# Kernel tuning notes

Hardware: AMD Instinct MI355X
Metric: run time of the kernel (lower is better)

## Reference

```python
import jax, jax.numpy as jnp
import numpy as np

B = 32768          # RL batch (many parallel env steps)
N = 12             # robot graph nodes (1 torso + 11 joint nodes)
D = 64             # node embedding dim
TORSO_DIM = 6
JOINT_DIM = 2
N_JOINTS = 11
OBS_DIM = TORSO_DIM + N_JOINTS * JOINT_DIM  # 28


def _build_adj_norm():
    # Ant-like tree: torso node 0, four legs of ~3 nodes each; edge_index was
    # built with self_loop=True and GCNConv uses add_self_loops=False, so we
    # symmetric-normalize (A + I).
    A = np.zeros((N, N), np.float32)
    edges = [(0, 1), (1, 2), (2, 3), (0, 4), (4, 5), (5, 6),
             (0, 7), (7, 8), (8, 9), (0, 10), (10, 11)]
    for i, j in edges:
        A[i, j] = 1.0
        A[j, i] = 1.0
    A += np.eye(N, dtype=np.float32)
    dinv = 1.0 / np.sqrt(A.sum(1))
    return jnp.asarray(A * dinv[:, None] * dinv[None, :])


def setup_inputs() -> dict:
    key = jax.random.key(0)
    ks = jax.random.split(key, 12)

    def w(k, shape):
        fan_in = shape[0]
        return jax.random.normal(k, shape, jnp.float32) / np.sqrt(fan_in)

    return {
        "observations": jax.random.normal(ks[0], (B, OBS_DIM), jnp.float32),
        "adj_norm": _build_adj_norm(),
        "w_in_torso": w(ks[1], (TORSO_DIM, D)), "b_in_torso": jnp.zeros((D,), jnp.float32),
        "w_in_joint": w(ks[2], (JOINT_DIM, D)), "b_in_joint": jnp.zeros((D,), jnp.float32),
        "w_gp1": w(ks[3], (D, D)), "b_gp1": jnp.zeros((D,), jnp.float32),
        "w_gp2": w(ks[4], (D, D)), "b_gp2": jnp.zeros((D,), jnp.float32),
        "w_gv1": w(ks[5], (D, D)), "b_gv1": jnp.zeros((D,), jnp.float32),
        "w_gv2": w(ks[6], (D, D)), "b_gv2": jnp.zeros((D,), jnp.float32),
        "w_pol1": w(ks[7], (D, D)), "b_pol1": jnp.zeros((D,), jnp.float32),
        "w_pol2": w(ks[8], (D, 1)), "b_pol2": jnp.zeros((1,), jnp.float32),
        "w_val1": w(ks[9], (N * D, D)), "b_val1": jnp.zeros((D,), jnp.float32),
        "w_val2": w(ks[10], (D, 1)), "b_val2": jnp.zeros((1,), jnp.float32),
    }


def reference(observations, adj_norm,
              w_in_torso, b_in_torso, w_in_joint, b_in_joint,
              w_gp1, b_gp1, w_gp2, b_gp2,
              w_gv1, b_gv1, w_gv2, b_gv2,
              w_pol1, b_pol1, w_pol2, b_pol2,
              w_val1, b_val1, w_val2, b_val2):
    b = observations.shape[0]
    # --- masked per-group node embedding (input model) ---
    obs_torso = observations[:, :TORSO_DIM]                              # [B,6]
    obs_joint = observations[:, TORSO_DIM:].reshape(b, N_JOINTS, JOINT_DIM)
    emb_t = jnp.tanh(obs_torso @ w_in_torso + b_in_torso)[:, None, :]    # [B,1,D]
    emb_j = jnp.tanh(jnp.einsum('bnf,fd->bnd', obs_joint, w_in_joint) + b_in_joint)
    x = jnp.concatenate([emb_t, emb_j], axis=1)                          # [B,N,D]

    # --- propagation model: GCNConv(x) = A_norm @ (x W) + b ---
    def gcn(h, W, bias):
        return jnp.einsum('nm,bmd->bnd', adj_norm, h @ W) + bias

    xp = jnp.tanh(gcn(x, w_gp1, b_gp1))
    xp = jnp.tanh(gcn(xp, w_gp2, b_gp2))                                 # policy GNN
    xv = jnp.tanh(gcn(x, w_gv1, b_gv1))
    xv = jnp.tanh(gcn(xv, w_gv2, b_gv2))                                 # value GNN

    # --- policy heads: one scalar per action (joint) node, shared group net ---
    act_emb = xp[:, 1:, :]                                               # [B,11,D]
    h = jnp.tanh(act_emb @ w_pol1 + b_pol1)
    latent_pi = (h @ w_pol2 + b_pol2)[..., 0]                            # [B,11]

    # --- value head: flatten all node embeddings ---
    flat = xv.reshape(b, N * D)                                          # [B,768]
    hv = jnp.tanh(flat @ w_val1 + b_val1)
    latent_vf = hv @ w_val2 + b_val2                                     # [B,1]
    return latent_pi, latent_vf
```

## Files before the change

### kernel.cpp

```cpp
#include <hip/hip_runtime.h>

#define NB 32768
#define NN 12
#define DD 64
#define OBSD 28
#define EPB 16
#define NSLOT 136

typedef __bf16 bf16x8 __attribute__((ext_vector_type(8)));
typedef __bf16 bf16x4 __attribute__((ext_vector_type(4)));
typedef __bf16 bf16x2 __attribute__((ext_vector_type(2)));
typedef float  f32x4  __attribute__((ext_vector_type(4)));

#define MFMA(a, b, c) __builtin_amdgcn_mfma_f32_16x16x32_bf16((a), (b), (c), 0, 0, 0)

__device__ __forceinline__ float tanh_fast(float x) {
    float e = __builtin_amdgcn_exp2f(x * 2.885390081777927f);
    float r = __builtin_amdgcn_rcpf(e + 1.f);
    return __builtin_fmaf(-2.f, r, 1.f);
}

static constexpr int AC_OFF[13] = {0,5,8,11,13,16,19,21,24,27,29,32,34};
static constexpr int AC_M[34] = {0,1,4,7,10, 0,1,2, 1,2,3, 2,3, 0,4,5, 4,5,6, 5,6, 0,7,8, 7,8,9, 8,9, 0,10,11, 10,11};
static constexpr int AC_N[34] = {0,0,0,0,0, 1,1,1, 2,2,2, 3,3, 4,4,4, 5,5,5, 6,6, 7,7,7, 8,8,8, 9,9, 10,10,10, 11,11};

__global__ __launch_bounds__(256) void prep_weights(
    const float* __restrict__ gp1, const float* __restrict__ gp2,
    const float* __restrict__ gv1, const float* __restrict__ gv2,
    const float* __restrict__ pol1, const float* __restrict__ val1,
    __bf16* __restrict__ wsb)
{
    int gid = blockIdx.x * blockDim.x + threadIdx.x;
    if (gid >= NSLOT * 64) return;
    int slot = gid >> 6, l = gid & 63;
    const float* W; int w, ks;
    if (slot < 32) {
        int m = slot >> 3;
        W = (m == 0) ? gp1 : (m == 1) ? gp2 : (m == 2) ? gv1 : gv2;
        w = (slot >> 1) & 3; ks = slot & 1;
    } else if (slot < 40) {
        W = pol1; w = (slot - 32) >> 1; ks = slot & 1;
    } else {
        int idx = slot - 40; W = val1; w = idx / 24; ks = idx % 24;
    }
    int dout = w * 16 + (l & 15);
    int k0 = ks * 32 + (l >> 4) * 8;
    bf16x8 v;
    #pragma unroll
    for (int i = 0; i < 8; ++i) v[i] = (__bf16)W[(size_t)(k0 + i) * 64 + dout];
    *(bf16x8*)(wsb + (size_t)gid * 8) = v;
}

__global__ __launch_bounds__(512, 6) void nervenet_mfma(
    const float* __restrict__ obs, const float* __restrict__ adjn,
    const float* __restrict__ w_in_t, const float* __restrict__ b_in_t,
    const float* __restrict__ w_in_j, const float* __restrict__ b_in_j,
    const float* __restrict__ b_gp1, const float* __restrict__ b_gp2,
    const float* __restrict__ b_gv1, const float* __restrict__ b_gv2,
    const float* __restrict__ b_pol1, const float* __restrict__ w_pol2, const float* __restrict__ b_pol2,
    const float* __restrict__ b_val1, const float* __restrict__ w_val2, const float* __restrict__ b_val2,
    const __bf16* __restrict__ wsb, float* __restrict__ out)
{
    __shared__ unsigned char X [NN * EPB * DD * 2];
    __shared__ unsigned char XP[NN * EPB * DD * 2];
    __shared__ float polp[4 * 11 * EPB];
    __shared__ float valp[4 * EPB];

    const int tid = threadIdx.x;
    const int l   = tid & 63;
    const int el  = l & 15;
    const int kg  = l >> 4;
    const int wv  = tid >> 6;
    const int w   = wv & 3;
    const bool isP = wv < 4;
    const int b0  = blockIdx.x * EPB;
    const int swz = (el & 7) << 4;

    float ac[34];
    #pragma unroll
    for (int i = 0; i < 34; ++i) ac[i] = adjn[AC_N[i] * 12 + AC_M[i]];

    {
        const int ee = tid & 15, fg = tid >> 4;
        const int eswz = (ee & 7) << 4;
        const float* os = obs + (size_t)(b0 + ee) * OBSD;
        f32x4 o0 = *(const f32x4*)(os);
        f32x4 o1 = *(const f32x4*)(os + 4);
        f32x4 o2 = *(const f32x4*)(os + 8);
        f32x4 o3 = *(const f32x4*)(os + 12);
        f32x4 o4 = *(const f32x4*)(os + 16);
        f32x4 o5 = *(const f32x4*)(os + 20);
        f32x4 o6 = *(const f32x4*)(os + 24);
        float tors[6] = {o0[0], o0[1], o0[2], o0[3], o1[0], o1[1]};
        float j0[11] = {o1[2], o2[0], o2[2], o3[0], o3[2], o4[0], o4[2], o5[0], o5[2], o6[0], o6[2]};
        float j1[11] = {o1[3], o2[1], o2[3], o3[1], o3[3], o4[1], o4[3], o5[1], o5[3], o6[1], o6[3]};

        float y0 = b_in_t[fg * 2], y1 = b_in_t[fg * 2 + 1];
        #pragma unroll
        for (int ff = 0; ff < 6; ++ff) {
            y0 = __builtin_fmaf(tors[ff], w_in_t[ff * DD + fg * 2], y0);
            y1 = __builtin_fmaf(tors[ff], w_in_t[ff * DD + fg * 2 + 1], y1);
        }
        bf16x2 t;
        t[0] = (__bf16)tanh_fast(y0); t[1] = (__bf16)tanh_fast(y1);
        *(bf16x2*)(&X[(0 * EPB + ee) * 128 + ((fg * 4) ^ eswz)]) = t;

        const float wj0a = w_in_j[fg * 2], wj0b = w_in_j[fg * 2 + 1];
        const float wj1a = w_in_j[DD + fg * 2], wj1b = w_in_j[DD + fg * 2 + 1];
        const float bja = b_in_j[fg * 2], bjb = b_in_j[fg * 2 + 1];
        #pragma unroll
        for (int n = 1; n < NN; ++n) {
            float ya = __builtin_fmaf(j1[n-1], wj1a, __builtin_fmaf(j0[n-1], wj0a, bja));
            float yb = __builtin_fmaf(j1[n-1], wj1b, __builtin_fmaf(j0[n-1], wj0b, bjb));
            t[0] = (__bf16)tanh_fast(ya); t[1] = (__bf16)tanh_fast(yb);
            *(bf16x2*)(&X[(n * EPB + ee) * 128 + ((fg * 4) ^ eswz)]) = t;
        }
    }

    auto rdfrag = [&](const unsigned char* buf, int n, int ks) {
        return *(const bf16x8*)(buf + (n * EPB + el) * 128 + ((ks * 64 + kg * 16) ^ swz));
    };
    auto ldws = [&](int slot) {
        return *(const bf16x8*)(wsb + ((size_t)slot * 64 + l) * 8);
    };

    f32x4 acc[NN];

    auto gcn_read = [&](const unsigned char* src, int slotbase) {
        bf16x8 wf0 = ldws(slotbase + w * 2 + 0);
        bf16x8 wf1 = ldws(slotbase + w * 2 + 1);
        #pragma unroll
        for (int n = 0; n < NN; ++n) {
            bf16x8 x0 = rdfrag(src, n, 0);
            bf16x8 x1 = rdfrag(src, n, 1);
            f32x4 a = {0.f, 0.f, 0.f, 0.f};
            a = MFMA(wf0, x0, a);
            a = MFMA(wf1, x1, a);
            acc[n] = a;
        }
    };
    auto gcn_write = [&](unsigned char* dst, const float* bias) {
        f32x4 bv = *(const f32x4*)(bias + w * 16 + kg * 4);
        #pragma unroll
        for (int n = 0; n < NN; ++n) {
            f32x4 y = bv;
            #pragma unroll
            for (int j = AC_OFF[n]; j < AC_OFF[n + 1]; ++j) {
                const float a = ac[j];
                #pragma unroll
                for (int r = 0; r < 4; ++r) y[r] = __builtin_fmaf(a, acc[AC_M[j]][r], y[r]);
            }
            bf16x4 o;
            #pragma unroll
            for (int r = 0; r < 4; ++r) o[r] = (__bf16)tanh_fast(y[r]);
            *(bf16x4*)(dst + (n * EPB + el) * 128 + (((w * 16 + kg * 4) * 2) ^ swz)) = o;
        }
    };

    unsigned char* MYBUF = isP ? XP : X;

    __syncthreads();
    gcn_read(X, isP ? 0 : 16);
    __syncthreads();
    gcn_write(MYBUF, isP ? b_gp1 : b_gv1);
    __syncthreads();
    gcn_read(MYBUF, isP ? 8 : 24);
    __syncthreads();
    gcn_write(MYBUF, isP ? b_gp2 : b_gv2);
    __syncthreads();

    {
        f32x4 bp  = *(const f32x4*)(b_pol1 + w * 16 + kg * 4);
        f32x4 wp2 = *(const f32x4*)(w_pol2 + w * 16 + kg * 4);
        bf16x8 pf0 = ldws(32 + w * 2 + 0);
        bf16x8 pf1 = ldws(32 + w * 2 + 1);
        auto pol_unit = [&](int nj) {
            bf16x8 x0 = rdfrag(XP, nj + 1, 0);
            bf16x8 x1 = rdfrag(XP, nj + 1, 1);
            f32x4 a = bp;
            a = MFMA(pf0, x0, a);
            a = MFMA(pf1, x1, a);
            float p = 0.f;
            #pragma unroll
            for (int r = 0; r < 4; ++r) p += tanh_fast(a[r]) * wp2[r];
            p += __shfl_xor(p, 16);
            p += __shfl_xor(p, 32);
            if (kg == 0) polp[w * 176 + nj * 16 + el] = p;
        };
        if (isP) {
            #pragma unroll
            for (int nj = 0; nj < 7; ++nj) pol_unit(nj);
        } else {
            #pragma unroll
            for (int nj = 7; nj < 11; ++nj) pol_unit(nj);
            f32x4 a0 = *(const f32x4*)(b_val1 + w * 16 + kg * 4);
            f32x4 a1 = {0.f, 0.f, 0.f, 0.f};
            #pragma unroll 4
            for (int ks = 0; ks < 24; ks += 2) {
                bf16x8 wf0 = ldws(40 + w * 24 + ks);
                bf16x8 wf1 = ldws(40 + w * 24 + ks + 1);
                int n = ks >> 1;
                bf16x8 xf0 = rdfrag(X, n, 0);
                bf16x8 xf1 = rdfrag(X, n, 1);
                a0 = MFMA(wf0, xf0, a0);
                a1 = MFMA(wf1, xf1, a1);
            }
            f32x4 wv2 = *(const f32x4*)(w_val2 + w * 16 + kg * 4);
            float p = 0.f;
            #pragma unroll
            for (int r = 0; r < 4; ++r) p += tanh_fast(a0[r] + a1[r]) * wv2[r];
            p += __shfl_xor(p, 16);
            p += __shfl_xor(p, 32);
            if (kg == 0) valp[w * 16 + el] = p;
        }
    }
    __syncthreads();

    if (tid < 176) {
        int e2 = tid / 11, nj = tid - e2 * 11;
        out[(size_t)b0 * 11 + tid] =
            polp[nj * 16 + e2] + polp[176 + nj * 16 + e2] +
            polp[352 + nj * 16 + e2] + polp[528 + nj * 16 + e2] + b_pol2[0];
    }
    if (tid >= 192 && tid < 192 + EPB) {
        int e2 = tid - 192;
        out[(size_t)NB * 11 + b0 + e2] =
            valp[e2] + valp[16 + e2] + valp[32 + e2] + valp[48 + e2] + b_val2[0];
    }
}

extern "C" void kernel_launch(void* const* d_in, const int* in_sizes, int n_in,
                              void* d_out, int out_size, void* d_ws, size_t ws_size,
                              hipStream_t stream) {
    (void)in_sizes; (void)n_in; (void)out_size; (void)ws_size;
    const float** p = (const float**)d_in;
    __bf16* wsb = (__bf16*)d_ws;
    hipLaunchKernelGGL(prep_weights, dim3(34), dim3(256), 0, stream,
        p[6], p[8], p[10], p[12], p[14], p[18], wsb);
    hipLaunchKernelGGL(nervenet_mfma, dim3(NB / EPB), dim3(512), 0, stream,
        p[0], p[1], p[2], p[3], p[4], p[5],
        p[7], p[9], p[11], p[13],
        p[15], p[16], p[17],
        p[19], p[20], p[21],
        wsb, (float*)d_out);
}
```

Measured before the change: 61.17 us.

## Hoist GCN weight/bias loads, use packed FMA, reorder LDS to env-major layout

Moves the GCN weight fragment and bias loads to kernel start so their global latency overlaps the embedding phase. Rewrites the embedding and GCN aggregation arithmetic with two-wide float vectors so the compiler can emit packed FMA instructions. Changes the shared-memory node layout from node-major to environment-major, with base pointers precomputed per lane. In exchange it holds more registers live across the embedding phase, which could lower occupancy.

New measurement: 63.20 us. 1.03x slower.

```diff
diff --git a/kernel.cpp b/kernel.cpp
--- a/kernel.cpp
+++ b/kernel.cpp
@@ -11,6 +11,7 @@
 typedef __bf16 bf16x4 __attribute__((ext_vector_type(4)));
 typedef __bf16 bf16x2 __attribute__((ext_vector_type(2)));
 typedef float  f32x4  __attribute__((ext_vector_type(4)));
+typedef float  f32x2  __attribute__((ext_vector_type(2)));
 
 #define MFMA(a, b, c) __builtin_amdgcn_mfma_f32_16x16x32_bf16((a), (b), (c), 0, 0, 0)
 
@@ -61,8 +62,8 @@
     const float* __restrict__ b_val1, const float* __restrict__ w_val2, const float* __restrict__ b_val2,
     const __bf16* __restrict__ wsb, float* __restrict__ out)
 {
-    __shared__ unsigned char X [NN * EPB * DD * 2];
-    __shared__ unsigned char XP[NN * EPB * DD * 2];
+    __shared__ unsigned char X [EPB * NN * DD * 2];
+    __shared__ unsigned char XP[EPB * NN * DD * 2];
     __shared__ float polp[4 * 11 * EPB];
     __shared__ float valp[4 * EPB];
 
@@ -76,6 +77,21 @@
     const int b0  = blockIdx.x * EPB;
     const int swz = (el & 7) << 4;
 
+    auto ldws = [&](int slot) {
+        return *(const bf16x8*)(wsb + ((size_t)slot * 64 + l) * 8);
+    };
+
+    const int sb1 = isP ? 0 : 16;
+    const int sb2 = isP ? 8 : 24;
+    const float* bias1 = isP ? b_gp1 : b_gv1;
+    const float* bias2 = isP ? b_gp2 : b_gv2;
+    bf16x8 wfA0 = ldws(sb1 + w * 2), wfA1 = ldws(sb1 + w * 2 + 1);
+    bf16x8 wfB0 = ldws(sb2 + w * 2), wfB1 = ldws(sb2 + w * 2 + 1);
+    f32x2 bA0 = *(const f32x2*)(bias1 + w * 16 + kg * 4);
+    f32x2 bA1 = *(const f32x2*)(bias1 + w * 16 + kg * 4 + 2);
+    f32x2 bB0 = *(const f32x2*)(bias2 + w * 16 + kg * 4);
+    f32x2 bB1 = *(const f32x2*)(bias2 + w * 16 + kg * 4 + 2);
+
     float ac[34];
     #pragma unroll
     for (int i = 0; i < 34; ++i) ac[i] = adjn[AC_N[i] * 12 + AC_M[i]];
@@ -83,6 +99,7 @@
     {
         const int ee = tid & 15, fg = tid >> 4;
         const int eswz = (ee & 7) << 4;
+        unsigned char* wp = X + (ee * NN) * 128 + ((fg * 4) ^ eswz);
         const float* os = obs + (size_t)(b0 + ee) * OBSD;
         f32x4 o0 = *(const f32x4*)(os);
         f32x4 o1 = *(const f32x4*)(os + 4);
@@ -95,40 +112,37 @@
         float j0[11] = {o1[2], o2[0], o2[2], o3[0], o3[2], o4[0], o4[2], o5[0], o5[2], o6[0], o6[2]};
         float j1[11] = {o1[3], o2[1], o2[3], o3[1], o3[3], o4[1], o4[3], o5[1], o5[3], o6[1], o6[3]};
 
-        float y0 = b_in_t[fg * 2], y1 = b_in_t[fg * 2 + 1];
-        #pragma unroll
-        for (int ff = 0; ff < 6; ++ff) {
-            y0 = __builtin_fmaf(tors[ff], w_in_t[ff * DD + fg * 2], y0);
-            y1 = __builtin_fmaf(tors[ff], w_in_t[ff * DD + fg * 2 + 1], y1);
-        }
-        bf16x2 t;
-        t[0] = (__bf16)tanh_fast(y0); t[1] = (__bf16)tanh_fast(y1);
-        *(bf16x2*)(&X[(0 * EPB + ee) * 128 + ((fg * 4) ^ eswz)]) = t;
-
-        const float wj0a = w_in_j[fg * 2], wj0b = w_in_j[fg * 2 + 1];
-        const float wj1a = w_in_j[DD + fg * 2], wj1b = w_in_j[DD + fg * 2 + 1];
-        const float bja = b_in_j[fg * 2], bjb = b_in_j[fg * 2 + 1];
+        f32x2 y = *(const f32x2*)(b_in_t + fg * 2);
+        #pragma unroll
+        for (int t = 0; t < 6; ++t) {
+            f32x2 ob = {tors[t], tors[t]};
+            y = __builtin_elementwise_fma(ob, *(const f32x2*)(w_in_t + t * DD + fg * 2), y);
+        }
+        bf16x2 t2;
+        t2[0] = (__bf16)tanh_fast(y[0]); t2[1] = (__bf16)tanh_fast(y[1]);
+        *(bf16x2*)(wp) = t2;
+
+        f32x2 wj0 = *(const f32x2*)(w_in_j + fg * 2);
+        f32x2 wj1 = *(const f32x2*)(w_in_j + DD + fg * 2);
+        f32x2 bj  = *(const f32x2*)(b_in_j + fg * 2);
         #pragma unroll
         for (int n = 1; n < NN; ++n) {
-            float ya = __builtin_fmaf(j1[n-1], wj1a, __builtin_fmaf(j0[n-1], wj0a, bja));
-            float yb = __builtin_fmaf(j1[n-1], wj1b, __builtin_fmaf(j0[n-1], wj0b, bjb));
-            t[0] = (__bf16)tanh_fast(ya); t[1] = (__bf16)tanh_fast(yb);
-            *(bf16x2*)(&X[(n * EPB + ee) * 128 + ((fg * 4) ^ eswz)]) = t;
+            f32x2 a0 = {j0[n - 1], j0[n - 1]};
+            f32x2 a1 = {j1[n - 1], j1[n - 1]};
+            f32x2 yn = __builtin_elementwise_fma(a1, wj1,
+                        __builtin_elementwise_fma(a0, wj0, bj));
+            t2[0] = (__bf16)tanh_fast(yn[0]); t2[1] = (__bf16)tanh_fast(yn[1]);
+            *(bf16x2*)(wp + n * 128) = t2;
         }
     }
 
     auto rdfrag = [&](const unsigned char* buf, int n, int ks) {
-        return *(const bf16x8*)(buf + (n * EPB + el) * 128 + ((ks * 64 + kg * 16) ^ swz));
-    };
-    auto ldws = [&](int slot) {
-        return *(const bf16x8*)(wsb + ((size_t)slot * 64 + l) * 8);
+        return *(const bf16x8*)(buf + (el * NN + n) * 128 + ((ks * 64 + kg * 16) ^ swz));
     };
 
     f32x4 acc[NN];
 
-    auto gcn_read = [&](const unsigned char* src, int slotbase) {
-        bf16x8 wf0 = ldws(slotbase + w * 2 + 0);
-        bf16x8 wf1 = ldws(slotbase + w * 2 + 1);
+    auto gcn_read = [&](const unsigned char* src, bf16x8 wf0, bf16x8 wf1) {
         #pragma unroll
         for (int n = 0; n < NN; ++n) {
             bf16x8 x0 = rdfrag(src, n, 0);
@@ -139,34 +153,38 @@
             acc[n] = a;
         }
     };
-    auto gcn_write = [&](unsigned char* dst, const float* bias) {
-        f32x4 bv = *(const f32x4*)(bias + w * 16 + kg * 4);
+    auto gcn_write = [&](unsigned char* dst, f32x2 bv0, f32x2 bv1) {
+        unsigned char* rowp = dst + (el * NN) * 128 + (((w * 16 + kg * 4) * 2) ^ swz);
         #pragma unroll
         for (int n = 0; n < NN; ++n) {
-            f32x4 y = bv;
+            f32x2 y0 = bv0, y1 = bv1;
             #pragma unroll
             for (int j = AC_OFF[n]; j < AC_OFF[n + 1]; ++j) {
                 const float a = ac[j];
-                #pragma unroll
-                for (int r = 0; r < 4; ++r) y[r] = __builtin_fmaf(a, acc[AC_M[j]][r], y[r]);
+                f32x2 a2 = {a, a};
+                const int m = AC_M[j];
+                f32x2 lo = __builtin_shufflevector(acc[m], acc[m], 0, 1);
+                f32x2 hi = __builtin_shufflevector(acc[m], acc[m], 2, 3);
+                y0 = __builtin_elementwise_fma(a2, lo, y0);
+                y1 = __builtin_elementwise_fma(a2, hi, y1);
             }
             bf16x4 o;
-            #pragma unroll
-            for (int r = 0; r < 4; ++r) o[r] = (__bf16)tanh_fast(y[r]);
-            *(bf16x4*)(dst + (n * EPB + el) * 128 + (((w * 16 + kg * 4) * 2) ^ swz)) = o;
+            o[0] = (__bf16)tanh_fast(y0[0]); o[1] = (__bf16)tanh_fast(y0[1]);
+            o[2] = (__bf16)tanh_fast(y1[0]); o[3] = (__bf16)tanh_fast(y1[1]);
+            *(bf16x4*)(rowp + n * 128) = o;
         }
     };
 
     unsigned char* MYBUF = isP ? XP : X;
 
     __syncthreads();
-    gcn_read(X, isP ? 0 : 16);
-    __syncthreads();
-    gcn_write(MYBUF, isP ? b_gp1 : b_gv1);
-    __syncthreads();
-    gcn_read(MYBUF, isP ? 8 : 24);
-    __syncthreads();
-    gcn_write(MYBUF, isP ? b_gp2 : b_gv2);
+    gcn_read(X, wfA0, wfA1);
+    __syncthreads();
+    gcn_write(MYBUF, bA0, bA1);
+    __syncthreads();
+    gcn_read(MYBUF, wfB0, wfB1);
+    __syncthreads();
+    gcn_write(MYBUF, bB0, bB1);
     __syncthreads();
 
     {
```
